# Kernel optimization log

Measured on AMD Instinct MI355X. Metric: run time of the kernel, lower is better.

The kernel has to match this reference:

```python
import jax, jax.numpy as jnp
import numpy as np

N_NODES = 100000
N_EDGES = 1600000
IN_CH, HID_CH, OUT_CH = 128, 64, 64


def setup_inputs() -> dict:
    key = jax.random.key(0)
    ks = jax.random.split(key, 9)
    def glorot(k, shape):
        lim = jnp.sqrt(6.0 / (shape[0] + shape[1]))
        return jax.random.uniform(k, shape, jnp.float32, -lim, lim)
    return {
        "x": jax.random.normal(ks[0], (N_NODES, IN_CH), jnp.float32),
        "edge_src": jax.random.randint(ks[1], (N_EDGES,), 0, N_NODES, jnp.int32),
        "edge_dst": jax.random.randint(ks[2], (N_EDGES,), 0, N_NODES, jnp.int32),
        "W1": glorot(ks[3], (IN_CH, HID_CH)),
        "b1": jnp.zeros((HID_CH,), jnp.float32),
        "W2": glorot(ks[4], (HID_CH, HID_CH)),
        "b2": jnp.zeros((HID_CH,), jnp.float32),
        "W3": glorot(ks[5], (HID_CH, OUT_CH)),
        "b3": jnp.zeros((OUT_CH,), jnp.float32),
    }


def _gcn_layer(h, W, b, edge_src, edge_dst):
    # GCNConv(normalize=False): transform then sum-aggregate over incoming edges
    hw = h @ W                                   # [N, d_out]
    msg = hw[edge_src]                           # [E, d_out] gather
    agg = jax.ops.segment_sum(msg, edge_dst, num_segments=N_NODES)  # scatter-add
    return agg + b


def reference(x, edge_src, edge_dst, W1, b1, W2, b2, W3, b3):
    # layer 1 + relu (dropout is identity at inference)
    h = jax.nn.relu(_gcn_layer(x, W1, b1, edge_src, edge_dst))
    # layer 2 + relu
    h = jax.nn.relu(_gcn_layer(h, W2, b2, edge_src, edge_dst))
    # final layer, no activation
    return _gcn_layer(h, W3, b3, edge_src, edge_dst)
```

## Files before the change

### kernel.cpp

```cpp
#include <hip/hip_runtime.h>

#define CH 64
#define BNODES 128
#define NB_MAX 1024
#define CUR_PAD 16
#define SCAT_CHUNK 8192
#define SCAT_THREADS 1024
#define BSLACK 1024
#define HIST_BLOCKS 256

typedef unsigned short ushort_t;
typedef unsigned int uint_t;
typedef short short8_t __attribute__((ext_vector_type(8)));
typedef float float4_t __attribute__((ext_vector_type(4)));

static __device__ __forceinline__ ushort_t f2bf(float x) {
    uint_t u = __float_as_uint(x);
    u = (u + 0x7FFFu + ((u >> 16) & 1u)) >> 16;
    return (ushort_t)u;
}
static __device__ __forceinline__ float bflo(uint_t u) {
    return __uint_as_float(u << 16);
}
static __device__ __forceinline__ float bfhi(uint_t u) {
    return __uint_as_float(u & 0xFFFF0000u);
}

__global__ __launch_bounds__(256) void prep_kernel(
    const float* __restrict__ W1, const float* __restrict__ W2, const float* __restrict__ W3,
    ushort_t* __restrict__ Wt1, ushort_t* __restrict__ Wt2, ushort_t* __restrict__ Wt3,
    int* __restrict__ bcnt, int NB)
{
    const int b = blockIdx.x;
    if (b == 3) {
        for (int i = threadIdx.x; i < NB; i += 256) bcnt[i] = 0;
        return;
    }
    const float* W = (b == 0) ? W1 : (b == 1) ? W2 : W3;
    ushort_t* Wt   = (b == 0) ? Wt1 : (b == 1) ? Wt2 : Wt3;
    const int K    = (b == 0) ? 128 : 64;
    for (int i = threadIdx.x; i < K * CH; i += 256) {
        int n = i / K, k = i % K;
        Wt[i] = f2bf(W[(size_t)k * CH + n]);
    }
}

template<int K, typename T>
static __device__ __forceinline__ void gemm_body(
    const T* __restrict__ h, const ushort_t* __restrict__ Wt,
    ushort_t* __restrict__ outb, int n, ushort_t* Hs, int blockRow)
{
    constexpr int LDH = K + 8;
    constexpr int C8  = K / 8;
    constexpr int KC  = K / 32;

    const int t    = threadIdx.x;
    const int lane = t & 63;
    const int wv   = t >> 6;
    const int l15  = lane & 15;
    const int quad = lane >> 4;
    const int row0 = blockRow * 128;

    short8_t bfrag[4][KC];
    #pragma unroll
    for (int nt = 0; nt < 4; ++nt)
        #pragma unroll
        for (int kc = 0; kc < KC; ++kc)
            bfrag[nt][kc] = *(const short8_t*)(Wt + (size_t)(nt * 16 + l15) * K + kc * 32 + quad * 8);

    for (int idx = t; idx < 128 * C8; idx += 256) {
        int r  = idx / C8;
        int c8 = idx % C8;
        int rg = row0 + r;
        short8_t v = (short8_t)0;
        if (rg < n) {
            if constexpr (sizeof(T) == 4) {
                const float* p = (const float*)h + (size_t)rg * K + c8 * 8;
                float4 f0 = *(const float4*)p;
                float4 f1 = *(const float4*)(p + 4);
                v[0] = (short)f2bf(f0.x); v[1] = (short)f2bf(f0.y);
                v[2] = (short)f2bf(f0.z); v[3] = (short)f2bf(f0.w);
                v[4] = (short)f2bf(f1.x); v[5] = (short)f2bf(f1.y);
                v[6] = (short)f2bf(f1.z); v[7] = (short)f2bf(f1.w);
            } else {
                v = *(const short8_t*)((const ushort_t*)h + (size_t)rg * K + c8 * 8);
            }
        }
        *(short8_t*)&Hs[r * LDH + c8 * 8] = v;
    }
    __syncthreads();

    float4_t acc[2][4];
    #pragma unroll
    for (int mi = 0; mi < 2; ++mi)
        #pragma unroll
        for (int nt = 0; nt < 4; ++nt)
            acc[mi][nt] = (float4_t)0.f;

    #pragma unroll
    for (int kc = 0; kc < KC; ++kc) {
        short8_t a0 = *(const short8_t*)&Hs[(wv * 32 +      l15) * LDH + kc * 32 + quad * 8];
        short8_t a1 = *(const short8_t*)&Hs[(wv * 32 + 16 + l15) * LDH + kc * 32 + quad * 8];
        #pragma unroll
        for (int nt = 0; nt < 4; ++nt) {
            acc[0][nt] = __builtin_amdgcn_mfma_f32_16x16x32_bf16(a0, bfrag[nt][kc], acc[0][nt], 0, 0, 0);
            acc[1][nt] = __builtin_amdgcn_mfma_f32_16x16x32_bf16(a1, bfrag[nt][kc], acc[1][nt], 0, 0, 0);
        }
    }

    #pragma unroll
    for (int mi = 0; mi < 2; ++mi) {
        #pragma unroll
        for (int r = 0; r < 4; ++r) {
            int row = row0 + wv * 32 + mi * 16 + quad * 4 + r;
            if (row <= n) {
                #pragma unroll
                for (int nt = 0; nt < 4; ++nt)
                    outb[(size_t)row * CH + nt * 16 + l15] = f2bf(acc[mi][nt][r]);
            }
        }
    }
}

template<int K, typename T>
__global__ __launch_bounds__(256) void gemm_mfma(
    const T* __restrict__ h, const ushort_t* __restrict__ Wt,
    ushort_t* __restrict__ outb, int n)
{
    __shared__ ushort_t Hs[128 * (K + 8)];
    gemm_body<K, T>(h, Wt, outb, n, Hs, blockIdx.x);
}

__global__ __launch_bounds__(256) void gemm1_hist(
    const float* __restrict__ x, const ushort_t* __restrict__ Wt1,
    ushort_t* __restrict__ outb, int n,
    const int* __restrict__ dst, int* __restrict__ bcnt, int E, int NB, int gemmGrid)
{
    __shared__ ushort_t Hs[128 * 136];
    if (blockIdx.x >= gemmGrid) {
        int* h = (int*)Hs;
        const int t = threadIdx.x;
        for (int i = t; i < NB; i += 256) h[i] = 0;
        __syncthreads();
        for (int i = (blockIdx.x - gemmGrid) * 256 + t; i < E; i += HIST_BLOCKS * 256)
            atomicAdd(&h[dst[i] >> 7], 1);
        __syncthreads();
        for (int i = t; i < NB; i += 256) {
            int v = h[i];
            if (v) atomicAdd(&bcnt[i], v);
        }
        return;
    }
    gemm_body<128, float>(x, Wt1, outb, n, Hs, blockIdx.x);
}

__global__ __launch_bounds__(256) void bucket_scan(
    const int* __restrict__ bcnt, int* __restrict__ boff,
    int* __restrict__ cursor, int NB)
{
    __shared__ int tsum[256];
    int t = threadIdx.x;
    int base = t * 4;
    int c[4];
    #pragma unroll
    for (int j = 0; j < 4; ++j) {
        int i = base + j;
        c[j] = (i < NB) ? bcnt[i] : 0;
    }
    int local = c[0] + c[1] + c[2] + c[3];
    tsum[t] = local;
    __syncthreads();
    for (int off = 1; off < 256; off <<= 1) {
        int v = (t >= off) ? tsum[t - off] : 0;
        __syncthreads();
        tsum[t] += v;
        __syncthreads();
    }
    int p = tsum[t] - local;
    #pragma unroll
    for (int j = 0; j < 4; ++j) {
        int i = base + j;
        if (i < NB) { boff[i] = p; cursor[i * CUR_PAD] = p; }
        p += c[j];
    }
    if (t == 255) boff[NB] = tsum[255];
}

__global__ __launch_bounds__(SCAT_THREADS) void bucket_scatter_blk(
    const int* __restrict__ src, const int* __restrict__ dst,
    int* __restrict__ cursor, int* __restrict__ bucketed, int E, int NB)
{
    __shared__ int hist[NB_MAX];
    __shared__ int rbase[NB_MAX];
    __shared__ int lcur[NB_MAX];

    const int t = threadIdx.x;
    const int s = blockIdx.x * SCAT_CHUNK;
    const int e = min(s + SCAT_CHUNK, E);

    for (int i = t; i < NB; i += SCAT_THREADS) hist[i] = 0;
    __syncthreads();

    for (int i = s + t; i < e; i += SCAT_THREADS)
        atomicAdd(&hist[dst[i] >> 7], 1);
    __syncthreads();

    for (int i = t; i < NB; i += SCAT_THREADS) {
        int c = hist[i];
        rbase[i] = c ? atomicAdd(&cursor[i * CUR_PAD], c) : 0;
        lcur[i] = 0;
    }
    __syncthreads();

    for (int i = s + t; i < e; i += SCAT_THREADS) {
        int d = dst[i];
        int b = d >> 7;
        int p = atomicAdd(&lcur[b], 1);
        bucketed[rbase[b] + p] = ((d & 127) << 17) | src[i];
    }
}

__global__ __launch_bounds__(256) void node_sort(
    const int* __restrict__ bucketed, const int* __restrict__ boff,
    int* __restrict__ sorted_src, int2* __restrict__ seg, int N, int zrow)
{
    __shared__ int cnt[BNODES];
    __shared__ int sc[BNODES];
    __shared__ int cur[BNODES];
    const int bk = blockIdx.x;
    const int t  = threadIdx.x;
    const int s  = boff[bk];
    const int e  = boff[bk + 1];
    const int sbase = (s + bk * BSLACK + 7) & ~7;

    if (t < BNODES) cnt[t] = 0;
    __syncthreads();
    for (int i = s + t; i < e; i += 256)
        atomicAdd(&cnt[((unsigned)bucketed[i]) >> 17], 1);
    __syncthreads();

    int pc = 0;
    if (t < BNODES) { pc = (cnt[t] + 7) & ~7; sc[t] = pc; }
    __syncthreads();
    for (int o = 1; o < BNODES; o <<= 1) {
        int v = (t < BNODES && t >= o) ? sc[t - o] : 0;
        __syncthreads();
        if (t < BNODES) sc[t] += v;
        __syncthreads();
    }
    if (t < BNODES) {
        int pexcl = sc[t] - pc;
        cur[t] = pexcl;
        int node = bk * BNODES + t;
        if (node < N) seg[node] = make_int2(sbase + pexcl, pc);
        for (int k = cnt[t]; k < pc; ++k)
            sorted_src[sbase + pexcl + k] = zrow << 3;
    }
    __syncthreads();

    for (int i = s + t; i < e; i += 256) {
        int p = bucketed[i];
        int d = ((unsigned)p) >> 17;
        int pos = atomicAdd(&cur[d], 1);
        sorted_src[sbase + pos] = (p & 0x1FFFF) << 3;
    }
}

template<bool BF16_RELU_OUT>
__global__ __launch_bounds__(256) void aggregate_kernel(
    const ushort_t* __restrict__ hwb, const int* __restrict__ sorted_src,
    const int2* __restrict__ seg, const float* __restrict__ bias,
    ushort_t* __restrict__ outb, float* __restrict__ outf, int N)
{
    const int t    = threadIdx.x;
    const int lane = t & 63;
    const int node = blockIdx.x * 4 + (t >> 6);
    if (node >= N) return;

    int2 scv  = seg[node];
    int  base = __builtin_amdgcn_readfirstlane(scv.x);
    int  pc   = __builtin_amdgcn_readfirstlane(scv.y);

    const int g = lane >> 3;
    const int c = lane & 7;
    const uint4* hw4 = (const uint4*)hwb;
    const int*   sp  = sorted_src + base;

    float a0 = 0.f, a1 = 0.f, a2 = 0.f, a3 = 0.f;
    float a4 = 0.f, a5 = 0.f, a6 = 0.f, a7 = 0.f;

    int u = 0;
    for (; u + 16 <= pc; u += 16) {
        int r0 = sp[u +     g];
        int r1 = sp[u + 8 + g];
        uint4 v0 = hw4[(size_t)(r0 + c)];
        uint4 v1 = hw4[(size_t)(r1 + c)];
        a0 += bflo(v0.x); a1 += bfhi(v0.x); a2 += bflo(v0.y); a3 += bfhi(v0.y);
        a4 += bflo(v0.z); a5 += bfhi(v0.z); a6 += bflo(v0.w); a7 += bfhi(v0.w);
        a0 += bflo(v1.x); a1 += bfhi(v1.x); a2 += bflo(v1.y); a3 += bfhi(v1.y);
        a4 += bflo(v1.z); a5 += bfhi(v1.z); a6 += bflo(v1.w); a7 += bfhi(v1.w);
    }
    if (u < pc) {
        int r0 = sp[u + g];
        uint4 v0 = hw4[(size_t)(r0 + c)];
        a0 += bflo(v0.x); a1 += bfhi(v0.x); a2 += bflo(v0.y); a3 += bfhi(v0.y);
        a4 += bflo(v0.z); a5 += bfhi(v0.z); a6 += bflo(v0.w); a7 += bfhi(v0.w);
    }

    a0 += __shfl_xor(a0, 8);  a1 += __shfl_xor(a1, 8);
    a2 += __shfl_xor(a2, 8);  a3 += __shfl_xor(a3, 8);
    a4 += __shfl_xor(a4, 8);  a5 += __shfl_xor(a5, 8);
    a6 += __shfl_xor(a6, 8);  a7 += __shfl_xor(a7, 8);
    a0 += __shfl_xor(a0, 16); a1 += __shfl_xor(a1, 16);
    a2 += __shfl_xor(a2, 16); a3 += __shfl_xor(a3, 16);
    a4 += __shfl_xor(a4, 16); a5 += __shfl_xor(a5, 16);
    a6 += __shfl_xor(a6, 16); a7 += __shfl_xor(a7, 16);
    a0 += __shfl_xor(a0, 32); a1 += __shfl_xor(a1, 32);
    a2 += __shfl_xor(a2, 32); a3 += __shfl_xor(a3, 32);
    a4 += __shfl_xor(a4, 32); a5 += __shfl_xor(a5, 32);
    a6 += __shfl_xor(a6, 32); a7 += __shfl_xor(a7, 32);

    float4 bv0 = *(const float4*)(bias + 8 * c);
    float4 bv1 = *(const float4*)(bias + 8 * c + 4);
    a0 += bv0.x; a1 += bv0.y; a2 += bv0.z; a3 += bv0.w;
    a4 += bv1.x; a5 += bv1.y; a6 += bv1.z; a7 += bv1.w;

    if (lane < 8) {
        if (BF16_RELU_OUT) {
            uint4 o;
            o.x = (uint_t)f2bf(fmaxf(a0, 0.f)) | ((uint_t)f2bf(fmaxf(a1, 0.f)) << 16);
            o.y = (uint_t)f2bf(fmaxf(a2, 0.f)) | ((uint_t)f2bf(fmaxf(a3, 0.f)) << 16);
            o.z = (uint_t)f2bf(fmaxf(a4, 0.f)) | ((uint_t)f2bf(fmaxf(a5, 0.f)) << 16);
            o.w = (uint_t)f2bf(fmaxf(a6, 0.f)) | ((uint_t)f2bf(fmaxf(a7, 0.f)) << 16);
            ((uint4*)outb)[(size_t)node * 8 + c] = o;
        } else {
            *(float4*)(outf + (size_t)node * CH + 8 * c)     = make_float4(a0, a1, a2, a3);
            *(float4*)(outf + (size_t)node * CH + 8 * c + 4) = make_float4(a4, a5, a6, a7);
        }
    }
}

extern "C" void kernel_launch(void* const* d_in, const int* in_sizes, int n_in,
                              void* d_out, int out_size, void* d_ws, size_t ws_size,
                              hipStream_t stream) {
    const float* x    = (const float*)d_in[0];
    const int*   esrc = (const int*)  d_in[1];
    const int*   edst = (const int*)  d_in[2];
    const float* W1   = (const float*)d_in[3];
    const float* b1   = (const float*)d_in[4];
    const float* W2   = (const float*)d_in[5];
    const float* b2   = (const float*)d_in[6];
    const float* W3   = (const float*)d_in[7];
    const float* b3   = (const float*)d_in[8];
    float* out = (float*)d_out;

    const int N  = in_sizes[0] / 128;
    const int E  = in_sizes[1];
    const int NB = (N + BNODES - 1) / BNODES;

    char* ws = (char*)d_ws;
    ushort_t* hwb   = (ushort_t*)ws; ws += (size_t)(N + 1) * CH * 2;
    ushort_t* hb    = (ushort_t*)ws; ws += (size_t)N * CH * 2;
    int* bucketed   = (int*)ws;      ws += (size_t)E * 4;
    ws = (char*)(((uintptr_t)ws + 15) & ~(uintptr_t)15);
    int* sorted_src = (int*)ws;      ws += ((size_t)E + (size_t)NB * BSLACK + 64) * 4;
    int2* seg       = (int2*)ws;     ws += (size_t)N * 8;
    int* bcnt       = (int*)ws;      ws += (size_t)NB * 4;
    int* boff       = (int*)ws;      ws += (size_t)(NB + 1) * 4;
    ws = (char*)(((uintptr_t)ws + 63) & ~(uintptr_t)63);
    int* cursor     = (int*)ws;      ws += (size_t)NB * CUR_PAD * 4;
    ws = (char*)(((uintptr_t)ws + 15) & ~(uintptr_t)15);
    ushort_t* Wt1   = (ushort_t*)ws; ws += (size_t)CH * 128 * 2;
    ushort_t* Wt2   = (ushort_t*)ws; ws += (size_t)CH * 64 * 2;
    ushort_t* Wt3   = (ushort_t*)ws; ws += (size_t)CH * 64 * 2;

    dim3 blk(256);
    int gemmGrid = (N + 1 + 127) / 128;
    int aggGrid  = (N + 3) / 4;
    int scatGrid = (E + SCAT_CHUNK - 1) / SCAT_CHUNK;

    prep_kernel<<<4, blk, 0, stream>>>(W1, W2, W3, Wt1, Wt2, Wt3, bcnt, NB);

    gemm1_hist<<<gemmGrid + HIST_BLOCKS, blk, 0, stream>>>(
        x, Wt1, hwb, N, edst, bcnt, E, NB, gemmGrid);

    bucket_scan<<<1, blk, 0, stream>>>(bcnt, boff, cursor, NB);
    bucket_scatter_blk<<<scatGrid, dim3(SCAT_THREADS), 0, stream>>>(esrc, edst, cursor, bucketed, E, NB);
    node_sort<<<NB, blk, 0, stream>>>(bucketed, boff, sorted_src, seg, N, N );

    aggregate_kernel<true><<<aggGrid, blk, 0, stream>>>(hwb, sorted_src, seg, b1, hb, nullptr, N);
    gemm_mfma<64, ushort_t><<<gemmGrid, blk, 0, stream>>>(hb, Wt2, hwb, N);
    aggregate_kernel<true><<<aggGrid, blk, 0, stream>>>(hwb, sorted_src, seg, b2, hb, nullptr, N);
    gemm_mfma<64, ushort_t><<<gemmGrid, blk, 0, stream>>>(hb, Wt3, hwb, N);
    aggregate_kernel<false><<<aggGrid, blk, 0, stream>>>(hwb, sorted_src, seg, b3, nullptr, out, N);
}
```

Baseline: 311.4 us.

## Store neighbor lists in fixed 32-slot per-node records with overflow array

Replaces the prefix-scanned CSR layout with a fixed-size record of 32 source indices per node, laid out transposed so each lane group loads an int4 of indices in one access. Nodes with more neighbors spill the remainder into an overflow array allocated by a global atomic. This removes the block scan in node_sort and the dependent index loads in the aggregate loop, letting up to four row gathers issue at once. In exchange it uses more memory for index records (N*32 ints) and adds branching in the aggregate kernel.

```diff
diff --git a/kernel.cpp b/kernel.cpp
--- a/kernel.cpp
+++ b/kernel.cpp
@@ -6,8 +6,8 @@
 #define CUR_PAD 16
 #define SCAT_CHUNK 8192
 #define SCAT_THREADS 1024
-#define BSLACK 1024
 #define HIST_BLOCKS 256
+#define REC 32
 
 typedef unsigned short ushort_t;
 typedef unsigned int uint_t;
@@ -29,11 +29,12 @@
 __global__ __launch_bounds__(256) void prep_kernel(
     const float* __restrict__ W1, const float* __restrict__ W2, const float* __restrict__ W3,
     ushort_t* __restrict__ Wt1, ushort_t* __restrict__ Wt2, ushort_t* __restrict__ Wt3,
-    int* __restrict__ bcnt, int NB)
+    int* __restrict__ bcnt, int* __restrict__ ovfcur, int NB)
 {
     const int b = blockIdx.x;
     if (b == 3) {
         for (int i = threadIdx.x; i < NB; i += 256) bcnt[i] = 0;
+        if (threadIdx.x == 0) *ovfcur = 0;
         return;
     }
     const float* W = (b == 0) ? W1 : (b == 1) ? W2 : W3;
@@ -222,53 +223,59 @@
 
 __global__ __launch_bounds__(256) void node_sort(
     const int* __restrict__ bucketed, const int* __restrict__ boff,
-    int* __restrict__ sorted_src, int2* __restrict__ seg, int N, int zrow)
+    int* __restrict__ fixedrec, int* __restrict__ ovf, int* __restrict__ ovfcur,
+    int2* __restrict__ seg, int* __restrict__ pcs, int N, int zrow)
 {
     __shared__ int cnt[BNODES];
-    __shared__ int sc[BNODES];
     __shared__ int cur[BNODES];
+    __shared__ int obase_sh[BNODES];
     const int bk = blockIdx.x;
     const int t  = threadIdx.x;
     const int s  = boff[bk];
     const int e  = boff[bk + 1];
-    const int sbase = (s + bk * BSLACK + 7) & ~7;
-
-    if (t < BNODES) cnt[t] = 0;
+
+    if (t < BNODES) { cnt[t] = 0; cur[t] = 0; }
     __syncthreads();
     for (int i = s + t; i < e; i += 256)
         atomicAdd(&cnt[((unsigned)bucketed[i]) >> 17], 1);
     __syncthreads();
 
-    int pc = 0;
-    if (t < BNODES) { pc = (cnt[t] + 7) & ~7; sc[t] = pc; }
-    __syncthreads();
-    for (int o = 1; o < BNODES; o <<= 1) {
-        int v = (t < BNODES && t >= o) ? sc[t - o] : 0;
-        __syncthreads();
-        if (t < BNODES) sc[t] += v;
-        __syncthreads();
-    }
     if (t < BNODES) {
-        int pexcl = sc[t] - pc;
-        cur[t] = pexcl;
         int node = bk * BNODES + t;
-        if (node < N) seg[node] = make_int2(sbase + pexcl, pc);
-        for (int k = cnt[t]; k < pc; ++k)
-            sorted_src[sbase + pexcl + k] = zrow << 3;
+        if (node < N) {
+            int ct = cnt[t];
+            int pcpad = (ct + 7) & ~7;
+            pcs[node] = pcpad;
+            int ob = 0;
+            if (pcpad > REC) {
+                ob = atomicAdd(ovfcur, pcpad - REC);
+                seg[node] = make_int2(ob, 0);
+            }
+            obase_sh[t] = ob;
+            int zv = zrow << 3;
+            for (int k = ct; k < pcpad; ++k) {
+                if (k < REC) fixedrec[node * REC + (k & 7) * 4 + (k >> 3)] = zv;
+                else         ovf[ob + k - REC] = zv;
+            }
+        }
     }
     __syncthreads();
 
     for (int i = s + t; i < e; i += 256) {
         int p = bucketed[i];
         int d = ((unsigned)p) >> 17;
-        int pos = atomicAdd(&cur[d], 1);
-        sorted_src[sbase + pos] = (p & 0x1FFFF) << 3;
+        int j = atomicAdd(&cur[d], 1);
+        int val = (p & 0x1FFFF) << 3;
+        int node = bk * BNODES + d;
+        if (j < REC) fixedrec[node * REC + (j & 7) * 4 + (j >> 3)] = val;
+        else         ovf[obase_sh[d] + j - REC] = val;
     }
 }
 
 template<bool BF16_RELU_OUT>
 __global__ __launch_bounds__(256) void aggregate_kernel(
-    const ushort_t* __restrict__ hwb, const int* __restrict__ sorted_src,
+    const ushort_t* __restrict__ hwb, const int* __restrict__ fixedrec,
+    const int* __restrict__ ovf, const int* __restrict__ pcs,
     const int2* __restrict__ seg, const float* __restrict__ bias,
     ushort_t* __restrict__ outb, float* __restrict__ outf, int N)
 {
@@ -277,34 +284,50 @@
     const int node = blockIdx.x * 4 + (t >> 6);
     if (node >= N) return;
 
-    int2 scv  = seg[node];
-    int  base = __builtin_amdgcn_readfirstlane(scv.x);
-    int  pc   = __builtin_amdgcn_readfirstlane(scv.y);
-
     const int g = lane >> 3;
     const int c = lane & 7;
     const uint4* hw4 = (const uint4*)hwb;
-    const int*   sp  = sorted_src + base;
+
+    int pcv = __builtin_amdgcn_readfirstlane(pcs[node]);
+    int4 ridx = ((const int4*)fixedrec)[node * (REC / 4) + g];
+
+    int pcc = pcv < REC ? pcv : REC;
 
     float a0 = 0.f, a1 = 0.f, a2 = 0.f, a3 = 0.f;
     float a4 = 0.f, a5 = 0.f, a6 = 0.f, a7 = 0.f;
 
-    int u = 0;
-    for (; u + 16 <= pc; u += 16) {
-        int r0 = sp[u +     g];
-        int r1 = sp[u + 8 + g];
-        uint4 v0 = hw4[(size_t)(r0 + c)];
-        uint4 v1 = hw4[(size_t)(r1 + c)];
+    uint4 v0, v1, v2, v3;
+    if (pcc > 0)  v0 = hw4[(size_t)(ridx.x + c)];
+    if (pcc > 8)  v1 = hw4[(size_t)(ridx.y + c)];
+    if (pcc > 16) v2 = hw4[(size_t)(ridx.z + c)];
+    if (pcc > 24) v3 = hw4[(size_t)(ridx.w + c)];
+
+    if (pcc > 0) {
         a0 += bflo(v0.x); a1 += bfhi(v0.x); a2 += bflo(v0.y); a3 += bfhi(v0.y);
         a4 += bflo(v0.z); a5 += bfhi(v0.z); a6 += bflo(v0.w); a7 += bfhi(v0.w);
+    }
+    if (pcc > 8) {
         a0 += bflo(v1.x); a1 += bfhi(v1.x); a2 += bflo(v1.y); a3 += bfhi(v1.y);
         a4 += bflo(v1.z); a5 += bfhi(v1.z); a6 += bflo(v1.w); a7 += bfhi(v1.w);
     }
-    if (u < pc) {
-        int r0 = sp[u + g];
-        uint4 v0 = hw4[(size_t)(r0 + c)];
-        a0 += bflo(v0.x); a1 += bfhi(v0.x); a2 += bflo(v0.y); a3 += bfhi(v0.y);
-        a4 += bflo(v0.z); a5 += bfhi(v0.z); a6 += bflo(v0.w); a7 += bfhi(v0.w);
+    if (pcc > 16) {
+        a0 += bflo(v2.x); a1 += bfhi(v2.x); a2 += bflo(v2.y); a3 += bfhi(v2.y);
+        a4 += bflo(v2.z); a5 += bfhi(v2.z); a6 += bflo(v2.w); a7 += bfhi(v2.w);
+    }
+    if (pcc > 24) {
+        a0 += bflo(v3.x); a1 += bfhi(v3.x); a2 += bflo(v3.y); a3 += bfhi(v3.y);
+        a4 += bflo(v3.z); a5 += bfhi(v3.z); a6 += bflo(v3.w); a7 += bfhi(v3.w);
+    }
+
+    if (pcv > REC) {
+        int ob = __builtin_amdgcn_readfirstlane(seg[node].x);
+        const int* op = ovf + ob;
+        for (int u = REC; u < pcv; u += 8) {
+            int r = op[u - REC + g];
+            uint4 v = hw4[(size_t)(r + c)];
+            a0 += bflo(v.x); a1 += bfhi(v.x); a2 += bflo(v.y); a3 += bfhi(v.y);
+            a4 += bflo(v.z); a5 += bfhi(v.z); a6 += bflo(v.w); a7 += bfhi(v.w);
+        }
     }
 
     a0 += __shfl_xor(a0, 8);  a1 += __shfl_xor(a1, 8);
@@ -363,12 +386,15 @@
     ushort_t* hb    = (ushort_t*)ws; ws += (size_t)N * CH * 2;
     int* bucketed   = (int*)ws;      ws += (size_t)E * 4;
     ws = (char*)(((uintptr_t)ws + 15) & ~(uintptr_t)15);
-    int* sorted_src = (int*)ws;      ws += ((size_t)E + (size_t)NB * BSLACK + 64) * 4;
+    int* fixedrec   = (int*)ws;      ws += (size_t)N * REC * 4;
+    int* ovf        = (int*)ws;      ws += (size_t)(E / 4 + 64) * 4;
     int2* seg       = (int2*)ws;     ws += (size_t)N * 8;
+    int* pcs        = (int*)ws;      ws += (size_t)N * 4;
     int* bcnt       = (int*)ws;      ws += (size_t)NB * 4;
     int* boff       = (int*)ws;      ws += (size_t)(NB + 1) * 4;
     ws = (char*)(((uintptr_t)ws + 63) & ~(uintptr_t)63);
     int* cursor     = (int*)ws;      ws += (size_t)NB * CUR_PAD * 4;
+    int* ovfcur     = (int*)ws;      ws += 64;
     ws = (char*)(((uintptr_t)ws + 15) & ~(uintptr_t)15);
     ushort_t* Wt1   = (ushort_t*)ws; ws += (size_t)CH * 128 * 2;
     ushort_t* Wt2   = (ushort_t*)ws; ws += (size_t)CH * 64 * 2;
@@ -379,18 +405,18 @@
     int aggGrid  = (N + 3) / 4;
     int scatGrid = (E + SCAT_CHUNK - 1) / SCAT_CHUNK;
 
-    prep_kernel<<<4, blk, 0, stream>>>(W1, W2, W3, Wt1, Wt2, Wt3, bcnt, NB);
+    prep_kernel<<<4, blk, 0, stream>>>(W1, W2, W3, Wt1, Wt2, Wt3, bcnt, ovfcur, NB);
 
     gemm1_hist<<<gemmGrid + HIST_BLOCKS, blk, 0, stream>>>(
         x, Wt1, hwb, N, edst, bcnt, E, NB, gemmGrid);
 
     bucket_scan<<<1, blk, 0, stream>>>(bcnt, boff, cursor, NB);
     bucket_scatter_blk<<<scatGrid, dim3(SCAT_THREADS), 0, stream>>>(esrc, edst, cursor, bucketed, E, NB);
-    node_sort<<<NB, blk, 0, stream>>>(bucketed, boff, sorted_src, seg, N, N );
-
-    aggregate_kernel<true><<<aggGrid, blk, 0, stream>>>(hwb, sorted_src, seg, b1, hb, nullptr, N);
+    node_sort<<<NB, blk, 0, stream>>>(bucketed, boff, fixedrec, ovf, ovfcur, seg, pcs, N, N );
+
+    aggregate_kernel<true><<<aggGrid, blk, 0, stream>>>(hwb, fixedrec, ovf, pcs, seg, b1, hb, nullptr, N);
     gemm_mfma<64, ushort_t><<<gemmGrid, blk, 0, stream>>>(hb, Wt2, hwb, N);
-    aggregate_kernel<true><<<aggGrid, blk, 0, stream>>>(hwb, sorted_src, seg, b2, hb, nullptr, N);
+    aggregate_kernel<true><<<aggGrid, blk, 0, stream>>>(hwb, fixedrec, ovf, pcs, seg, b2, hb, nullptr, N);
     gemm_mfma<64, ushort_t><<<gemmGrid, blk, 0, stream>>>(hb, Wt3, hwb, N);
-    aggregate_kernel<false><<<aggGrid, blk, 0, stream>>>(hwb, sorted_src, seg, b3, nullptr, out, N);
-}
+    aggregate_kernel<false><<<aggGrid, blk, 0, stream>>>(hwb, fixedrec, ovf, pcs, seg, b3, nullptr, out, N);
+}
```

Result: slower. 318.7 us (+2.3%).

## Fuse neighbor aggregation with the next layer's GEMM in one kernel

Applied to the files above, without the earlier changes.

Layers 1 and 2 now aggregate neighbor features, add bias, apply relu and run the next layer's 64x64 bf16 MFMA transform inside one kernel. The aggregated rows are staged in shared memory, so the separate GEMM launches and the full intermediate activation write and read-back are gone. Two ping-pong buffers replace the hb/hwb pair, and prep_kernel zeroes the padding row of the second buffer. In exchange, each block runs a 16-row MFMA on only 4 valid rows, reloads the weight fragments, waits at a block-wide barrier, and writes output with narrow 2-byte stores.

```diff
diff --git a/kernel.cpp b/kernel.cpp
--- a/kernel.cpp
+++ b/kernel.cpp
@@ -6,8 +6,8 @@
 #define CUR_PAD 16
 #define SCAT_CHUNK 8192
 #define SCAT_THREADS 1024
+#define HIST_BLOCKS 256
 #define BSLACK 1024
-#define HIST_BLOCKS 256
 
 typedef unsigned short ushort_t;
 typedef unsigned int uint_t;
@@ -29,11 +29,12 @@
 __global__ __launch_bounds__(256) void prep_kernel(
     const float* __restrict__ W1, const float* __restrict__ W2, const float* __restrict__ W3,
     ushort_t* __restrict__ Wt1, ushort_t* __restrict__ Wt2, ushort_t* __restrict__ Wt3,
-    int* __restrict__ bcnt, int NB)
+    int* __restrict__ bcnt, ushort_t* __restrict__ hwb2_zrow, int NB)
 {
     const int b = blockIdx.x;
     if (b == 3) {
         for (int i = threadIdx.x; i < NB; i += 256) bcnt[i] = 0;
+        if (threadIdx.x < CH) hwb2_zrow[threadIdx.x] = 0;
         return;
     }
     const float* W = (b == 0) ? W1 : (b == 1) ? W2 : W3;
@@ -122,15 +123,6 @@
     }
 }
 
-template<int K, typename T>
-__global__ __launch_bounds__(256) void gemm_mfma(
-    const T* __restrict__ h, const ushort_t* __restrict__ Wt,
-    ushort_t* __restrict__ outb, int n)
-{
-    __shared__ ushort_t Hs[128 * (K + 8)];
-    gemm_body<K, T>(h, Wt, outb, n, Hs, blockIdx.x);
-}
-
 __global__ __launch_bounds__(256) void gemm1_hist(
     const float* __restrict__ x, const ushort_t* __restrict__ Wt1,
     ushort_t* __restrict__ outb, int n,
@@ -266,29 +258,13 @@
     }
 }
 
-template<bool BF16_RELU_OUT>
-__global__ __launch_bounds__(256) void aggregate_kernel(
-    const ushort_t* __restrict__ hwb, const int* __restrict__ sorted_src,
-    const int2* __restrict__ seg, const float* __restrict__ bias,
-    ushort_t* __restrict__ outb, float* __restrict__ outf, int N)
-{
-    const int t    = threadIdx.x;
-    const int lane = t & 63;
-    const int node = blockIdx.x * 4 + (t >> 6);
-    if (node >= N) return;
-
-    int2 scv  = seg[node];
-    int  base = __builtin_amdgcn_readfirstlane(scv.x);
-    int  pc   = __builtin_amdgcn_readfirstlane(scv.y);
-
-    const int g = lane >> 3;
-    const int c = lane & 7;
-    const uint4* hw4 = (const uint4*)hwb;
-    const int*   sp  = sorted_src + base;
-
-    float a0 = 0.f, a1 = 0.f, a2 = 0.f, a3 = 0.f;
-    float a4 = 0.f, a5 = 0.f, a6 = 0.f, a7 = 0.f;
-
+static __device__ __forceinline__ void agg_core(
+    const uint4* __restrict__ hw4, const int* __restrict__ sorted_src,
+    int base, int pc, int g, int c,
+    float& a0, float& a1, float& a2, float& a3,
+    float& a4, float& a5, float& a6, float& a7)
+{
+    const int* sp = sorted_src + base;
     int u = 0;
     for (; u + 16 <= pc; u += 16) {
         int r0 = sp[u +     g];
@@ -319,24 +295,116 @@
     a2 += __shfl_xor(a2, 32); a3 += __shfl_xor(a3, 32);
     a4 += __shfl_xor(a4, 32); a5 += __shfl_xor(a5, 32);
     a6 += __shfl_xor(a6, 32); a7 += __shfl_xor(a7, 32);
-
-    float4 bv0 = *(const float4*)(bias + 8 * c);
-    float4 bv1 = *(const float4*)(bias + 8 * c + 4);
-    a0 += bv0.x; a1 += bv0.y; a2 += bv0.z; a3 += bv0.w;
-    a4 += bv1.x; a5 += bv1.y; a6 += bv1.z; a7 += bv1.w;
+}
+
+__global__ __launch_bounds__(256) void agg_gemm(
+    const ushort_t* __restrict__ hwb_in, const int* __restrict__ sorted_src,
+    const int2* __restrict__ seg, const float* __restrict__ bias,
+    const ushort_t* __restrict__ Wt, ushort_t* __restrict__ outb, int N)
+{
+    __shared__ ushort_t Hs[4 * 72];
+    const int t    = threadIdx.x;
+    const int lane = t & 63;
+    const int wv   = t >> 6;
+    const int node = blockIdx.x * 4 + wv;
+    const int g    = lane >> 3;
+    const int c    = lane & 7;
+    const uint4* hw4 = (const uint4*)hwb_in;
+
+    int base = 0, pc = 0;
+    if (node < N) {
+        int2 scv = seg[node];
+        base = __builtin_amdgcn_readfirstlane(scv.x);
+        pc   = __builtin_amdgcn_readfirstlane(scv.y);
+    }
+
+    float a0 = 0.f, a1 = 0.f, a2 = 0.f, a3 = 0.f;
+    float a4 = 0.f, a5 = 0.f, a6 = 0.f, a7 = 0.f;
+    agg_core(hw4, sorted_src, base, pc, g, c, a0, a1, a2, a3, a4, a5, a6, a7);
 
     if (lane < 8) {
-        if (BF16_RELU_OUT) {
-            uint4 o;
-            o.x = (uint_t)f2bf(fmaxf(a0, 0.f)) | ((uint_t)f2bf(fmaxf(a1, 0.f)) << 16);
-            o.y = (uint_t)f2bf(fmaxf(a2, 0.f)) | ((uint_t)f2bf(fmaxf(a3, 0.f)) << 16);
-            o.z = (uint_t)f2bf(fmaxf(a4, 0.f)) | ((uint_t)f2bf(fmaxf(a5, 0.f)) << 16);
-            o.w = (uint_t)f2bf(fmaxf(a6, 0.f)) | ((uint_t)f2bf(fmaxf(a7, 0.f)) << 16);
-            ((uint4*)outb)[(size_t)node * 8 + c] = o;
-        } else {
-            *(float4*)(outf + (size_t)node * CH + 8 * c)     = make_float4(a0, a1, a2, a3);
-            *(float4*)(outf + (size_t)node * CH + 8 * c + 4) = make_float4(a4, a5, a6, a7);
+        float4 bv0 = *(const float4*)(bias + 8 * c);
+        float4 bv1 = *(const float4*)(bias + 8 * c + 4);
+        a0 += bv0.x; a1 += bv0.y; a2 += bv0.z; a3 += bv0.w;
+        a4 += bv1.x; a5 += bv1.y; a6 += bv1.z; a7 += bv1.w;
+        uint4 o;
+        o.x = (uint_t)f2bf(fmaxf(a0, 0.f)) | ((uint_t)f2bf(fmaxf(a1, 0.f)) << 16);
+        o.y = (uint_t)f2bf(fmaxf(a2, 0.f)) | ((uint_t)f2bf(fmaxf(a3, 0.f)) << 16);
+        o.z = (uint_t)f2bf(fmaxf(a4, 0.f)) | ((uint_t)f2bf(fmaxf(a5, 0.f)) << 16);
+        o.w = (uint_t)f2bf(fmaxf(a6, 0.f)) | ((uint_t)f2bf(fmaxf(a7, 0.f)) << 16);
+        *(uint4*)&Hs[wv * 72 + c * 8] = o;
+    }
+    __syncthreads();
+
+    if (wv == 0) {
+        const int l15  = lane & 15;
+        const int quad = lane >> 4;
+
+        short8_t bfrag[4][2];
+        #pragma unroll
+        for (int nt = 0; nt < 4; ++nt)
+            #pragma unroll
+            for (int kc = 0; kc < 2; ++kc)
+                bfrag[nt][kc] = *(const short8_t*)(Wt + (size_t)(nt * 16 + l15) * 64 + kc * 32 + quad * 8);
+
+        short8_t afr[2];
+        #pragma unroll
+        for (int kc = 0; kc < 2; ++kc)
+            afr[kc] = (l15 < 4) ? *(const short8_t*)&Hs[l15 * 72 + kc * 32 + quad * 8]
+                                : (short8_t)0;
+
+        float4_t acc[4];
+        #pragma unroll
+        for (int nt = 0; nt < 4; ++nt) acc[nt] = (float4_t)0.f;
+        #pragma unroll
+        for (int kc = 0; kc < 2; ++kc)
+            #pragma unroll
+            for (int nt = 0; nt < 4; ++nt)
+                acc[nt] = __builtin_amdgcn_mfma_f32_16x16x32_bf16(afr[kc], bfrag[nt][kc], acc[nt], 0, 0, 0);
+
+        if (quad == 0) {
+            #pragma unroll
+            for (int r = 0; r < 4; ++r) {
+                int nd = blockIdx.x * 4 + r;
+                if (nd < N) {
+                    #pragma unroll
+                    for (int nt = 0; nt < 4; ++nt)
+                        outb[(size_t)nd * CH + nt * 16 + l15] = f2bf(acc[nt][r]);
+                }
+            }
         }
+    }
+}
+
+__global__ __launch_bounds__(256) void aggregate_final(
+    const ushort_t* __restrict__ hwb, const int* __restrict__ sorted_src,
+    const int2* __restrict__ seg, const float* __restrict__ bias,
+    float* __restrict__ outf, int N)
+{
+    const int t    = threadIdx.x;
+    const int lane = t & 63;
+    const int node = blockIdx.x * 4 + (t >> 6);
+    if (node >= N) return;
+
+    int2 scv  = seg[node];
+    int  base = __builtin_amdgcn_readfirstlane(scv.x);
+    int  pc   = __builtin_amdgcn_readfirstlane(scv.y);
+
+    const int g = lane >> 3;
+    const int c = lane & 7;
+    const uint4* hw4 = (const uint4*)hwb;
+
+    float a0 = 0.f, a1 = 0.f, a2 = 0.f, a3 = 0.f;
+    float a4 = 0.f, a5 = 0.f, a6 = 0.f, a7 = 0.f;
+    agg_core(hw4, sorted_src, base, pc, g, c, a0, a1, a2, a3, a4, a5, a6, a7);
+
+    if (lane < 8) {
+        float4 bv0 = *(const float4*)(bias + 8 * c);
+        float4 bv1 = *(const float4*)(bias + 8 * c + 4);
+        a0 += bv0.x; a1 += bv0.y; a2 += bv0.z; a3 += bv0.w;
+        a4 += bv1.x; a5 += bv1.y; a6 += bv1.z; a7 += bv1.w;
+        *(float4*)(outf + (size_t)node * CH + 8 * c)     = make_float4(a0, a1, a2, a3);
+        *(float4*)(outf + (size_t)node * CH + 8 * c + 4) = make_float4(a4, a5, a6, a7);
     }
 }
 
@@ -359,8 +427,8 @@
     const int NB = (N + BNODES - 1) / BNODES;
 
     char* ws = (char*)d_ws;
-    ushort_t* hwb   = (ushort_t*)ws; ws += (size_t)(N + 1) * CH * 2;
-    ushort_t* hb    = (ushort_t*)ws; ws += (size_t)N * CH * 2;
+    ushort_t* hwbA  = (ushort_t*)ws; ws += (size_t)(N + 1) * CH * 2;
+    ushort_t* hwbB  = (ushort_t*)ws; ws += (size_t)(N + 1) * CH * 2;
     int* bucketed   = (int*)ws;      ws += (size_t)E * 4;
     ws = (char*)(((uintptr_t)ws + 15) & ~(uintptr_t)15);
     int* sorted_src = (int*)ws;      ws += ((size_t)E + (size_t)NB * BSLACK + 64) * 4;
@@ -379,18 +447,17 @@
     int aggGrid  = (N + 3) / 4;
     int scatGrid = (E + SCAT_CHUNK - 1) / SCAT_CHUNK;
 
-    prep_kernel<<<4, blk, 0, stream>>>(W1, W2, W3, Wt1, Wt2, Wt3, bcnt, NB);
+    prep_kernel<<<4, blk, 0, stream>>>(W1, W2, W3, Wt1, Wt2, Wt3, bcnt,
+                                       hwbB + (size_t)N * CH, NB);
 
     gemm1_hist<<<gemmGrid + HIST_BLOCKS, blk, 0, stream>>>(
-        x, Wt1, hwb, N, edst, bcnt, E, NB, gemmGrid);
+        x, Wt1, hwbA, N, edst, bcnt, E, NB, gemmGrid);
 
     bucket_scan<<<1, blk, 0, stream>>>(bcnt, boff, cursor, NB);
     bucket_scatter_blk<<<scatGrid, dim3(SCAT_THREADS), 0, stream>>>(esrc, edst, cursor, bucketed, E, NB);
     node_sort<<<NB, blk, 0, stream>>>(bucketed, boff, sorted_src, seg, N, N );
 
-    aggregate_kernel<true><<<aggGrid, blk, 0, stream>>>(hwb, sorted_src, seg, b1, hb, nullptr, N);
-    gemm_mfma<64, ushort_t><<<gemmGrid, blk, 0, stream>>>(hb, Wt2, hwb, N);
-    aggregate_kernel<true><<<aggGrid, blk, 0, stream>>>(hwb, sorted_src, seg, b2, hb, nullptr, N);
-    gemm_mfma<64, ushort_t><<<gemmGrid, blk, 0, stream>>>(hb, Wt3, hwb, N);
-    aggregate_kernel<false><<<aggGrid, blk, 0, stream>>>(hwb, sorted_src, seg, b3, nullptr, out, N);
-}
+    agg_gemm<<<aggGrid, blk, 0, stream>>>(hwbA, sorted_src, seg, b1, Wt2, hwbB, N);
+    agg_gemm<<<aggGrid, blk, 0, stream>>>(hwbB, sorted_src, seg, b2, Wt3, hwbA, N);
+    aggregate_final<<<aggGrid, blk, 0, stream>>>(hwbA, sorted_src, seg, b3, out, N);
+}
```

Result: no change. 312.6 us (+0.4%).
